# Performance work log

Hardware: AMD Instinct MI355X
Metric: run time of the kernel (lower is better)

The kernel has to match this reference:

```python
import jax, jax.numpy as jnp
import numpy as np

N, E, D = 100000, 600000, 128
BN_EPS = 1e-5


def setup_inputs() -> dict:
    key = jax.random.key(0)
    ks = jax.random.split(key, 8)
    x = jax.random.normal(ks[0], (N, D), dtype=jnp.float32)
    edge_index = jax.random.randint(ks[1], (2, E), 0, N, dtype=jnp.int64)
    # learned params: GIN eps (train_eps=True, init 0), Linear-BN-Linear MLP
    eps = jnp.zeros((), dtype=jnp.float32)
    s = 1.0 / np.sqrt(D)
    W1 = jax.random.uniform(ks[2], (D, D), jnp.float32, -s, s)
    b1 = jax.random.uniform(ks[3], (D,), jnp.float32, -s, s)
    gamma = jnp.ones((D,), jnp.float32)
    beta = jnp.zeros((D,), jnp.float32)
    W2 = jax.random.uniform(ks[4], (D, D), jnp.float32, -s, s)
    b2 = jax.random.uniform(ks[5], (D,), jnp.float32, -s, s)
    return {"x": x, "edge_index": edge_index, "eps": eps, "W1": W1, "b1": b1,
            "gamma": gamma, "beta": beta, "W2": W2, "b2": b2}


def reference(x, edge_index, eps, W1, b1, gamma, beta, W2, b2):
    src, dst = edge_index[0], edge_index[1]
    n = x.shape[0]
    # GIN aggregation: sum of neighbor features scattered to target nodes
    agg = jax.ops.segment_sum(x[src], dst, num_segments=n)  # [N, D]
    h = (1.0 + eps) * x + agg
    # MLP: Linear -> BatchNorm1d (training-mode batch stats) -> ReLU -> Linear
    h = h @ W1.T + b1
    mean = jnp.mean(h, axis=0)
    var = jnp.mean(jnp.square(h - mean), axis=0)  # biased variance, as BN uses
    h = (h - mean) * jax.lax.rsqrt(var + BN_EPS) * gamma + beta
    h = jax.nn.relu(h)
    h = h @ W2.T + b2
    # outer residual with ReLU
    return x + jax.nn.relu(h)
```

## Files before the change

### kernel.cpp

```cpp
#include <hip/hip_runtime.h>
#include <hip/hip_bf16.h>


typedef __attribute__((ext_vector_type(8))) short short8;
typedef __attribute__((ext_vector_type(4))) float f32x4;

static __device__ __forceinline__ float bf2f(unsigned short u) {
    union { unsigned int i; float f; } z; z.i = ((unsigned int)u) << 16; return z.f;
}
static __device__ __forceinline__ unsigned short f2bf(float f) {
    unsigned int u = __float_as_uint(f);
    unsigned int lsb = (u >> 16) & 1u;
    u += 0x7fffu + lsb;
    return (unsigned short)(u >> 16);
}
static __device__ __forceinline__ void atomAdd(float* p, float v) {
    __hip_atomic_fetch_add(p, v, __ATOMIC_RELAXED, __HIP_MEMORY_SCOPE_AGENT);
}

__global__ __launch_bounds__(256) void k_detect(const unsigned short* __restrict__ gamma,
                                                const int* __restrict__ ei,
                                                int* __restrict__ flags,
                                                float* __restrict__ stats,
                                                int* __restrict__ counts, int N) {
    int idx = blockIdx.x * 256 + threadIdx.x;
    if (idx < N) counts[idx] = 0;
    if (blockIdx.x == 0) {
        int t = threadIdx.x;
        if (t < 256) stats[t] = 0.0f;
        if (t == 0) {
            flags[0] = (gamma[0] == 0x3F80u) ? 0 : 1;
            int odd = ei[1] | ei[3] | ei[5] | ei[7] | ei[9] | ei[11] | ei[13] | ei[15];
            flags[1] = (odd == 0) ? 1 : 0;
        }
    }
}

__global__ __launch_bounds__(256) void k_hist(const int* __restrict__ ei, int* __restrict__ counts,
                                              int E, const int* __restrict__ flags) {
    int e = blockIdx.x * 256 + threadIdx.x;
    if (e >= E) return;
    int dst = flags[1] ? ei[2 * E + 2 * e] : ei[E + e];
    atomicAdd(&counts[dst], 1);
}

__global__ __launch_bounds__(256) void k_scan1(const int* __restrict__ counts, int* __restrict__ partA,
                                               int N) {
    __shared__ int sd[256];
    int t = threadIdx.x, idx = blockIdx.x * 256 + t;
    sd[t] = (idx < N) ? counts[idx] : 0;
    __syncthreads();
    for (int off = 128; off > 0; off >>= 1) {
        if (t < off) sd[t] += sd[t + off];
        __syncthreads();
    }
    if (t == 0) partA[blockIdx.x] = sd[0];
}

__global__ __launch_bounds__(512) void k_scan2(const int* __restrict__ partA, int* __restrict__ partB,
                                               int NB) {
    __shared__ int sd[512];
    int t = threadIdx.x;
    sd[t] = (t < NB) ? partA[t] : 0;
    __syncthreads();
    for (int off = 1; off < 512; off <<= 1) {
        int v = (t >= off) ? sd[t - off] : 0;
        __syncthreads();
        sd[t] += v;
        __syncthreads();
    }
    if (t < NB) partB[t] = sd[t] - partA[t];
}

__global__ __launch_bounds__(256) void k_scan3(int* __restrict__ counts, int* __restrict__ rowptr,
                                               const int* __restrict__ partB, int N) {
    __shared__ int sd[256];
    int t = threadIdx.x, idx = blockIdx.x * 256 + t;
    int c = (idx < N) ? counts[idx] : 0;
    sd[t] = c;
    __syncthreads();
    for (int off = 1; off < 256; off <<= 1) {
        int v = (t >= off) ? sd[t - off] : 0;
        __syncthreads();
        sd[t] += v;
        __syncthreads();
    }
    int offB = partB[blockIdx.x];
    int excl = offB + sd[t] - c;
    if (idx < N) {
        rowptr[idx] = excl;
        counts[idx] = excl;
        if (idx == N - 1) rowptr[N] = excl + c;
    }
}

__global__ __launch_bounds__(256) void k_fill(const int* __restrict__ ei, int* __restrict__ cursor,
                                              int* __restrict__ bucket, int E,
                                              const int* __restrict__ flags) {
    int e = blockIdx.x * 256 + threadIdx.x;
    if (e >= E) return;
    int src, dst;
    if (flags[1]) { src = ei[2 * e]; dst = ei[2 * E + 2 * e]; }
    else          { src = ei[e];     dst = ei[E + e]; }
    int pos = atomicAdd(&cursor[dst], 1);
    bucket[pos] = src;
}

__global__ __launch_bounds__(256) void k_gather(const void* __restrict__ x,
                                                const void* __restrict__ eps,
                                                const int* __restrict__ rowptr,
                                                const int* __restrict__ bucket,
                                                unsigned int* __restrict__ h0, int N,
                                                const int* __restrict__ flags) {
    int wave = threadIdx.x >> 6, lane = threadIdx.x & 63;
    int n = blockIdx.x * 4 + wave;
    if (n >= N) return;
    int mode = flags[0];
    int beg = rowptr[n], end = rowptr[n + 1];
    float ax = 0.f, ay = 0.f;
    if (mode == 0) {
        const unsigned int* xr = (const unsigned int*)x;
        int e = beg;
        for (; e + 4 <= end; e += 4) {
            int s0 = bucket[e], s1 = bucket[e + 1], s2 = bucket[e + 2], s3 = bucket[e + 3];
            unsigned int u0 = xr[(size_t)s0 * 64 + lane];
            unsigned int u1 = xr[(size_t)s1 * 64 + lane];
            unsigned int u2 = xr[(size_t)s2 * 64 + lane];
            unsigned int u3 = xr[(size_t)s3 * 64 + lane];
            ax += (bf2f((unsigned short)(u0 & 0xffffu)) + bf2f((unsigned short)(u1 & 0xffffu)))
                + (bf2f((unsigned short)(u2 & 0xffffu)) + bf2f((unsigned short)(u3 & 0xffffu)));
            ay += (bf2f((unsigned short)(u0 >> 16)) + bf2f((unsigned short)(u1 >> 16)))
                + (bf2f((unsigned short)(u2 >> 16)) + bf2f((unsigned short)(u3 >> 16)));
        }
        if (e + 2 <= end) {
            int s0 = bucket[e], s1 = bucket[e + 1];
            unsigned int u0 = xr[(size_t)s0 * 64 + lane];
            unsigned int u1 = xr[(size_t)s1 * 64 + lane];
            ax += bf2f((unsigned short)(u0 & 0xffffu)) + bf2f((unsigned short)(u1 & 0xffffu));
            ay += bf2f((unsigned short)(u0 >> 16)) + bf2f((unsigned short)(u1 >> 16));
            e += 2;
        }
        if (e < end) {
            unsigned int u = xr[(size_t)bucket[e] * 64 + lane];
            ax += bf2f((unsigned short)(u & 0xffffu));
            ay += bf2f((unsigned short)(u >> 16));
        }
        float s = 1.0f + bf2f(((const unsigned short*)eps)[0]);
        unsigned int u = xr[(size_t)n * 64 + lane];
        ax = fmaf(s, bf2f((unsigned short)(u & 0xffffu)), ax);
        ay = fmaf(s, bf2f((unsigned short)(u >> 16)), ay);
    } else {
        const float2* xr = (const float2*)x;
        int e = beg;
        for (; e + 4 <= end; e += 4) {
            int s0 = bucket[e], s1 = bucket[e + 1], s2 = bucket[e + 2], s3 = bucket[e + 3];
            float2 v0 = xr[(size_t)s0 * 64 + lane];
            float2 v1 = xr[(size_t)s1 * 64 + lane];
            float2 v2 = xr[(size_t)s2 * 64 + lane];
            float2 v3 = xr[(size_t)s3 * 64 + lane];
            ax += (v0.x + v1.x) + (v2.x + v3.x);
            ay += (v0.y + v1.y) + (v2.y + v3.y);
        }
        for (; e < end; ++e) {
            float2 v = xr[(size_t)bucket[e] * 64 + lane];
            ax += v.x; ay += v.y;
        }
        float s = 1.0f + ((const float*)eps)[0];
        float2 v = xr[(size_t)n * 64 + lane];
        ax = fmaf(s, v.x, ax);
        ay = fmaf(s, v.y, ay);
    }
    h0[(size_t)n * 64 + lane] = (unsigned int)f2bf(ax) | ((unsigned int)f2bf(ay) << 16);
}

static __device__ __forceinline__ void stageW(const void* W, unsigned short* Wl,
                                              int tid, int mode) {
    for (int c = tid; c < 2048; c += 256) {
        int li = c & 15, kg = (c >> 4) & 15, t = c >> 8;
        int srcOff = (t * 16 + li) * 128 + kg * 8;
        if (mode == 0) {
            *(short8*)&Wl[c * 8] = *(const short8*)((const unsigned short*)W + srcOff);
        } else {
            const float4* wf = (const float4*)((const float*)W + srcOff);
            float4 f0 = wf[0], f1 = wf[1];
            union { short8 v; unsigned short s[8]; } u;
            u.s[0] = f2bf(f0.x); u.s[1] = f2bf(f0.y); u.s[2] = f2bf(f0.z); u.s[3] = f2bf(f0.w);
            u.s[4] = f2bf(f1.x); u.s[5] = f2bf(f1.y); u.s[6] = f2bf(f1.z); u.s[7] = f2bf(f1.w);
            *(short8*)&Wl[c * 8] = u.v;
        }
    }
}

__global__ __launch_bounds__(256, 4) void k_gemm1(const unsigned short* __restrict__ h0,
                                                  const void* __restrict__ W1,
                                                  const void* __restrict__ b1,
                                                  unsigned short* __restrict__ h1,
                                                  float* __restrict__ partials,
                                                  int N, const int* __restrict__ flags) {
    __shared__ unsigned short Wl[16384];
    __shared__ float bl[128];
    __shared__ float red_s[4][128], red_s2[4][128];
    int tid = threadIdx.x;
    int mode = flags[0];
    int lane = tid & 63, wave = tid >> 6;
    int li = lane & 15, q = lane >> 4;

    int m0 = blockIdx.x * 64 + wave * 16;
    int rowA = m0 + li; if (rowA >= N) rowA = N - 1;
    const unsigned short* ap = h0 + (size_t)rowA * 128 + q * 8;
    short8 av[4];
    av[0] = *(const short8*)(ap);
    av[1] = *(const short8*)(ap + 32);
    av[2] = *(const short8*)(ap + 64);
    av[3] = *(const short8*)(ap + 96);

    stageW(W1, Wl, tid, mode);
    if (tid < 128)
        bl[tid] = mode ? ((const float*)b1)[tid] : bf2f(((const unsigned short*)b1)[tid]);
    __syncthreads();

    f32x4 acc[8] = {};
#pragma unroll
    for (int c4 = 0; c4 < 4; ++c4) {
#pragma unroll
        for (int t = 0; t < 8; ++t) {
            short8 bfrag = *(const short8*)&Wl[(t * 256 + (c4 * 4 + q) * 16 + li) * 8];
            acc[t] = __builtin_amdgcn_mfma_f32_16x16x32_bf16(av[c4], bfrag, acc[t], 0, 0, 0);
        }
    }

    float s_acc[8] = {0.f, 0.f, 0.f, 0.f, 0.f, 0.f, 0.f, 0.f};
    float s2_acc[8] = {0.f, 0.f, 0.f, 0.f, 0.f, 0.f, 0.f, 0.f};
    bool full = (m0 + 16 <= N);
    if (full) {
        unsigned short* hp = h1 + (size_t)(m0 + q * 4) * 128 + li;
#pragma unroll
        for (int t = 0; t < 8; ++t) {
            float bb = bl[t * 16 + li];
#pragma unroll
            for (int r = 0; r < 4; ++r) {
                float v = acc[t][r] + bb;
                hp[(size_t)r * 128 + t * 16] = f2bf(v);
                s_acc[t] += v; s2_acc[t] += v * v;
            }
        }
    } else if (m0 < N) {
#pragma unroll
        for (int t = 0; t < 8; ++t) {
            int col = t * 16 + li;
            float bb = bl[col];
#pragma unroll
            for (int r = 0; r < 4; ++r) {
                int row = m0 + q * 4 + r;
                if (row < N) {
                    float v = acc[t][r] + bb;
                    h1[(size_t)row * 128 + col] = f2bf(v);
                    s_acc[t] += v; s2_acc[t] += v * v;
                }
            }
        }
    }
#pragma unroll
    for (int t = 0; t < 8; ++t) {
        float s = s_acc[t], s2 = s2_acc[t];
        s  += __shfl_xor(s, 16);  s  += __shfl_xor(s, 32);
        s2 += __shfl_xor(s2, 16); s2 += __shfl_xor(s2, 32);
        if (lane < 16) { red_s[wave][t * 16 + li] = s; red_s2[wave][t * 16 + li] = s2; }
    }
    __syncthreads();
    float pv;
    if (tid < 128) {
        pv = red_s[0][tid] + red_s[1][tid] + red_s[2][tid] + red_s[3][tid];
    } else {
        int c = tid - 128;
        pv = red_s2[0][c] + red_s2[1][c] + red_s2[2][c] + red_s2[3][c];
    }
    partials[(size_t)blockIdx.x * 256 + tid] = pv;
}

__global__ __launch_bounds__(256) void k_reduce(const float* __restrict__ partials,
                                                float* __restrict__ stats, int nb) {
    int t = threadIdx.x;
    float acc = 0.f;
    for (int b = blockIdx.x; b < nb; b += 64)
        acc += partials[(size_t)b * 256 + t];
    atomAdd(&stats[t], acc);
}

__global__ __launch_bounds__(256, 4) void k_gemm2(const unsigned short* __restrict__ h1,
                                                  const void* __restrict__ W2,
                                                  const void* __restrict__ b2,
                                                  const float* __restrict__ stats,
                                                  const void* __restrict__ gamma,
                                                  const void* __restrict__ beta,
                                                  const void* __restrict__ x,
                                                  void* __restrict__ out, int N, float invN,
                                                  const int* __restrict__ flags) {
    __shared__ unsigned short Wl[16384];
    __shared__ float bl[128], al[128], cl[128];
    int tid = threadIdx.x;
    int mode = flags[0];
    int lane = tid & 63, wave = tid >> 6;
    int li = lane & 15, q = lane >> 4;

    int m0 = blockIdx.x * 64 + wave * 16;
    int rowA = m0 + li; if (rowA >= N) rowA = N - 1;
    const unsigned short* ap = h1 + (size_t)rowA * 128 + q * 8;
    short8 hv[4];
    hv[0] = *(const short8*)(ap);
    hv[1] = *(const short8*)(ap + 32);
    hv[2] = *(const short8*)(ap + 64);
    hv[3] = *(const short8*)(ap + 96);

    stageW(W2, Wl, tid, mode);
    if (tid < 128) {
        bl[tid] = mode ? ((const float*)b2)[tid] : bf2f(((const unsigned short*)b2)[tid]);
        float mean = stats[tid] * invN;
        float var = stats[128 + tid] * invN - mean * mean;
        float g  = mode ? ((const float*)gamma)[tid] : bf2f(((const unsigned short*)gamma)[tid]);
        float bt = mode ? ((const float*)beta)[tid]  : bf2f(((const unsigned short*)beta)[tid]);
        float a = g * rsqrtf(var + 1e-5f);
        al[tid] = a;
        cl[tid] = bt - mean * a;
    }
    __syncthreads();

    short8 au[4];
#pragma unroll
    for (int c4 = 0; c4 < 4; ++c4) {
        int k0 = c4 * 32 + q * 8;
        union { short8 v; unsigned short s[8]; } hu; hu.v = hv[c4];
        float4 sa = *(const float4*)&al[k0];
        float4 sb = *(const float4*)&al[k0 + 4];
        float4 ca = *(const float4*)&cl[k0];
        float4 cb = *(const float4*)&cl[k0 + 4];
        union { short8 v; unsigned short s[8]; } uu;
        uu.s[0] = f2bf(fmaxf(fmaf(bf2f(hu.s[0]), sa.x, ca.x), 0.f));
        uu.s[1] = f2bf(fmaxf(fmaf(bf2f(hu.s[1]), sa.y, ca.y), 0.f));
        uu.s[2] = f2bf(fmaxf(fmaf(bf2f(hu.s[2]), sa.z, ca.z), 0.f));
        uu.s[3] = f2bf(fmaxf(fmaf(bf2f(hu.s[3]), sa.w, ca.w), 0.f));
        uu.s[4] = f2bf(fmaxf(fmaf(bf2f(hu.s[4]), sb.x, cb.x), 0.f));
        uu.s[5] = f2bf(fmaxf(fmaf(bf2f(hu.s[5]), sb.y, cb.y), 0.f));
        uu.s[6] = f2bf(fmaxf(fmaf(bf2f(hu.s[6]), sb.z, cb.z), 0.f));
        uu.s[7] = f2bf(fmaxf(fmaf(bf2f(hu.s[7]), sb.w, cb.w), 0.f));
        au[c4] = uu.v;
    }

    bool full = (m0 + 16 <= N);
    float xv[32];
    if (full) {
        if (mode == 0) {
            const unsigned short* xp = (const unsigned short*)x + (size_t)(m0 + q * 4) * 128 + li;
#pragma unroll
            for (int t = 0; t < 8; ++t)
#pragma unroll
                for (int r = 0; r < 4; ++r)
                    xv[t * 4 + r] = bf2f(xp[(size_t)r * 128 + t * 16]);
        } else {
            const float* xp = (const float*)x + (size_t)(m0 + q * 4) * 128 + li;
#pragma unroll
            for (int t = 0; t < 8; ++t)
#pragma unroll
                for (int r = 0; r < 4; ++r)
                    xv[t * 4 + r] = xp[(size_t)r * 128 + t * 16];
        }
    }

    f32x4 acc[8] = {};
#pragma unroll
    for (int c4 = 0; c4 < 4; ++c4) {
#pragma unroll
        for (int t = 0; t < 8; ++t) {
            short8 bfrag = *(const short8*)&Wl[(t * 256 + (c4 * 4 + q) * 16 + li) * 8];
            acc[t] = __builtin_amdgcn_mfma_f32_16x16x32_bf16(au[c4], bfrag, acc[t], 0, 0, 0);
        }
    }

    if (full) {
        if (mode == 0) {
            unsigned short* op = (unsigned short*)out + (size_t)(m0 + q * 4) * 128 + li;
#pragma unroll
            for (int t = 0; t < 8; ++t) {
                float bb = bl[t * 16 + li];
#pragma unroll
                for (int r = 0; r < 4; ++r)
                    op[(size_t)r * 128 + t * 16] =
                        f2bf(xv[t * 4 + r] + fmaxf(acc[t][r] + bb, 0.f));
            }
        } else {
            float* op = (float*)out + (size_t)(m0 + q * 4) * 128 + li;
#pragma unroll
            for (int t = 0; t < 8; ++t) {
                float bb = bl[t * 16 + li];
#pragma unroll
                for (int r = 0; r < 4; ++r)
                    op[(size_t)r * 128 + t * 16] =
                        xv[t * 4 + r] + fmaxf(acc[t][r] + bb, 0.f);
            }
        }
    } else if (m0 < N) {
#pragma unroll
        for (int t = 0; t < 8; ++t) {
            int col = t * 16 + li;
            float bb = bl[col];
#pragma unroll
            for (int r = 0; r < 4; ++r) {
                int row = m0 + q * 4 + r;
                if (row < N) {
                    size_t idx = (size_t)row * 128 + col;
                    float v = fmaxf(acc[t][r] + bb, 0.f);
                    if (mode == 0) {
                        float xvs = bf2f(((const unsigned short*)x)[idx]);
                        ((unsigned short*)out)[idx] = f2bf(xvs + v);
                    } else {
                        float xvs = ((const float*)x)[idx];
                        ((float*)out)[idx] = xvs + v;
                    }
                }
            }
        }
    }
}

extern "C" void kernel_launch(void* const* d_in, const int* in_sizes, int n_in,
                              void* d_out, int out_size, void* d_ws, size_t ws_size,
                              hipStream_t stream) {
    const void* x     = d_in[0];
    const int*  ei    = (const int*)d_in[1];
    const void* eps   = d_in[2];
    const void* W1    = d_in[3];
    const void* b1    = d_in[4];
    const void* gamma = d_in[5];
    const void* beta  = d_in[6];
    const void* W2    = d_in[7];
    const void* b2    = d_in[8];

    int N = in_sizes[0] / 128;
    int E = in_sizes[1] / 2;

    unsigned short* h0 = (unsigned short*)d_ws;
    unsigned short* h1 = h0 + (size_t)N * 128;
    int* counts = (int*)(h1 + (size_t)N * 128);
    int* rowptr = counts + N;
    int* bucket = rowptr + N + 1;
    int* partA  = bucket + E;
    int* partB  = partA + 512;
    float* stats = (float*)(partB + 512);
    int*   flags = (int*)(stats + 256);
    float* tail  = (float*)(flags + 16);

    int NB = (N + 255) / 256;
    int EB = (E + 255) / 256;
    int mb = (N + 63) / 64;

    size_t partials_elems = (size_t)mb * 256;
    size_t dead_elems = (size_t)N + (size_t)(N + 1) + (size_t)E;
    float* partials = (partials_elems <= dead_elems) ? (float*)counts : tail;

    k_detect<<<NB, 256, 0, stream>>>((const unsigned short*)gamma, ei, flags, stats, counts, N);
    k_hist<<<EB, 256, 0, stream>>>(ei, counts, E, flags);
    k_scan1<<<NB, 256, 0, stream>>>(counts, partA, N);
    k_scan2<<<1, 512, 0, stream>>>(partA, partB, NB);
    k_scan3<<<NB, 256, 0, stream>>>(counts, rowptr, partB, N);
    k_fill<<<EB, 256, 0, stream>>>(ei, counts, bucket, E, flags);

    k_gather<<<(N + 3) / 4, 256, 0, stream>>>(x, eps, rowptr, bucket,
                                              (unsigned int*)h0, N, flags);

    k_gemm1<<<mb, 256, 0, stream>>>(h0, W1, b1, h1, partials, N, flags);
    k_reduce<<<64, 256, 0, stream>>>(partials, stats, mb);
    k_gemm2<<<mb, 256, 0, stream>>>(h1, W2, b2, stats, gamma, beta, x, d_out, N,
                                    1.0f / (float)N, flags);
}
```

Measured before the change: 294.1 us.

## Split gather into column chunks with chunk-major h0 layout for gemm1

The gather kernel now has each wave handle 8 nodes, with 8 lanes per node covering one 16-column chunk, and a grid split across 8 column chunks. The intermediate h0 is written in a chunk-major layout, and gemm1 reads its A fragments from that layout. The aim is to raise memory-level parallelism and improve cache locality per column slice during the random neighbor gathers. In exchange, each gather load is only 32 bytes per node instead of a full row, and the edge index lists are re-read once per chunk.

Result: slower. 325.9 us (+10.8%).

```diff
diff --git a/kernel.cpp b/kernel.cpp
--- a/kernel.cpp
+++ b/kernel.cpp
@@ -110,67 +110,63 @@
                                                 const void* __restrict__ eps,
                                                 const int* __restrict__ rowptr,
                                                 const int* __restrict__ bucket,
-                                                unsigned int* __restrict__ h0, int N,
+                                                unsigned int* __restrict__ h0t, int N,
                                                 const int* __restrict__ flags) {
-    int wave = threadIdx.x >> 6, lane = threadIdx.x & 63;
-    int n = blockIdx.x * 4 + wave;
+    int tid = threadIdx.x;
+    int c = blockIdx.x & 7;
+    int nb = blockIdx.x >> 3;
+    int wave = tid >> 6, lane = tid & 63;
+    int g = lane >> 3, f = lane & 7;
+    int n = nb * 32 + wave * 8 + g;
     if (n >= N) return;
     int mode = flags[0];
     int beg = rowptr[n], end = rowptr[n + 1];
     float ax = 0.f, ay = 0.f;
     if (mode == 0) {
-        const unsigned int* xr = (const unsigned int*)x;
+        const unsigned int* xs = (const unsigned int*)x + c * 8 + f;
         int e = beg;
         for (; e + 4 <= end; e += 4) {
             int s0 = bucket[e], s1 = bucket[e + 1], s2 = bucket[e + 2], s3 = bucket[e + 3];
-            unsigned int u0 = xr[(size_t)s0 * 64 + lane];
-            unsigned int u1 = xr[(size_t)s1 * 64 + lane];
-            unsigned int u2 = xr[(size_t)s2 * 64 + lane];
-            unsigned int u3 = xr[(size_t)s3 * 64 + lane];
+            unsigned int u0 = xs[(size_t)s0 * 64];
+            unsigned int u1 = xs[(size_t)s1 * 64];
+            unsigned int u2 = xs[(size_t)s2 * 64];
+            unsigned int u3 = xs[(size_t)s3 * 64];
             ax += (bf2f((unsigned short)(u0 & 0xffffu)) + bf2f((unsigned short)(u1 & 0xffffu)))
                 + (bf2f((unsigned short)(u2 & 0xffffu)) + bf2f((unsigned short)(u3 & 0xffffu)));
             ay += (bf2f((unsigned short)(u0 >> 16)) + bf2f((unsigned short)(u1 >> 16)))
                 + (bf2f((unsigned short)(u2 >> 16)) + bf2f((unsigned short)(u3 >> 16)));
         }
-        if (e + 2 <= end) {
-            int s0 = bucket[e], s1 = bucket[e + 1];
-            unsigned int u0 = xr[(size_t)s0 * 64 + lane];
-            unsigned int u1 = xr[(size_t)s1 * 64 + lane];
-            ax += bf2f((unsigned short)(u0 & 0xffffu)) + bf2f((unsigned short)(u1 & 0xffffu));
-            ay += bf2f((unsigned short)(u0 >> 16)) + bf2f((unsigned short)(u1 >> 16));
-            e += 2;
-        }
-        if (e < end) {
-            unsigned int u = xr[(size_t)bucket[e] * 64 + lane];
+        for (; e < end; ++e) {
+            unsigned int u = xs[(size_t)bucket[e] * 64];
             ax += bf2f((unsigned short)(u & 0xffffu));
             ay += bf2f((unsigned short)(u >> 16));
         }
         float s = 1.0f + bf2f(((const unsigned short*)eps)[0]);
-        unsigned int u = xr[(size_t)n * 64 + lane];
+        unsigned int u = xs[(size_t)n * 64];
         ax = fmaf(s, bf2f((unsigned short)(u & 0xffffu)), ax);
         ay = fmaf(s, bf2f((unsigned short)(u >> 16)), ay);
     } else {
-        const float2* xr = (const float2*)x;
+        const float2* xs = (const float2*)x + c * 8 + f;
         int e = beg;
         for (; e + 4 <= end; e += 4) {
             int s0 = bucket[e], s1 = bucket[e + 1], s2 = bucket[e + 2], s3 = bucket[e + 3];
-            float2 v0 = xr[(size_t)s0 * 64 + lane];
-            float2 v1 = xr[(size_t)s1 * 64 + lane];
-            float2 v2 = xr[(size_t)s2 * 64 + lane];
-            float2 v3 = xr[(size_t)s3 * 64 + lane];
+            float2 v0 = xs[(size_t)s0 * 64];
+            float2 v1 = xs[(size_t)s1 * 64];
+            float2 v2 = xs[(size_t)s2 * 64];
+            float2 v3 = xs[(size_t)s3 * 64];
             ax += (v0.x + v1.x) + (v2.x + v3.x);
             ay += (v0.y + v1.y) + (v2.y + v3.y);
         }
         for (; e < end; ++e) {
-            float2 v = xr[(size_t)bucket[e] * 64 + lane];
+            float2 v = xs[(size_t)bucket[e] * 64];
             ax += v.x; ay += v.y;
         }
         float s = 1.0f + ((const float*)eps)[0];
-        float2 v = xr[(size_t)n * 64 + lane];
+        float2 v = xs[(size_t)n * 64];
         ax = fmaf(s, v.x, ax);
         ay = fmaf(s, v.y, ay);
     }
-    h0[(size_t)n * 64 + lane] = (unsigned int)f2bf(ax) | ((unsigned int)f2bf(ay) << 16);
+    h0t[((size_t)c * N + n) * 8 + f] = (unsigned int)f2bf(ax) | ((unsigned int)f2bf(ay) << 16);
 }
 
 static __device__ __forceinline__ void stageW(const void* W, unsigned short* Wl,
@@ -207,12 +203,14 @@
 
     int m0 = blockIdx.x * 64 + wave * 16;
     int rowA = m0 + li; if (rowA >= N) rowA = N - 1;
-    const unsigned short* ap = h0 + (size_t)rowA * 128 + q * 8;
+    size_t tstride = (size_t)N * 16;
+    int toff = (q & 1) * 8;
     short8 av[4];
-    av[0] = *(const short8*)(ap);
-    av[1] = *(const short8*)(ap + 32);
-    av[2] = *(const short8*)(ap + 64);
-    av[3] = *(const short8*)(ap + 96);
+#pragma unroll
+    for (int c4 = 0; c4 < 4; ++c4) {
+        av[c4] = *(const short8*)(h0 + (size_t)(2 * c4 + (q >> 1)) * tstride
+                                     + (size_t)rowA * 16 + toff);
+    }
 
     stageW(W1, Wl, tid, mode);
     if (tid < 128)
@@ -464,8 +462,9 @@
     k_scan3<<<NB, 256, 0, stream>>>(counts, rowptr, partB, N);
     k_fill<<<EB, 256, 0, stream>>>(ei, counts, bucket, E, flags);
 
-    k_gather<<<(N + 3) / 4, 256, 0, stream>>>(x, eps, rowptr, bucket,
-                                              (unsigned int*)h0, N, flags);
+    int gb = ((N + 31) / 32) * 8;
+    k_gather<<<gb, 256, 0, stream>>>(x, eps, rowptr, bucket,
+                                     (unsigned int*)h0, N, flags);
 
     k_gemm1<<<mb, 256, 0, stream>>>(h0, W1, b1, h1, partials, N, flags);
     k_reduce<<<64, 256, 0, stream>>>(partials, stats, mb);
```
